# Kernel optimization log

Measured on AMD Instinct MI355X. Metric: run time of the kernel, lower is better.

Reference implementation:

```python
import jax, jax.numpy as jnp
import numpy as np

N_NODES = 50000
N_EDGES = 1200000
F_IN = 128
HID = 64
N_CLASSES = 10
N_GRAPHS = 256
EPS = 1e-5


def setup_inputs() -> dict:
    key = jax.random.key(0)
    ks = jax.random.split(key, 12)
    x = jax.random.normal(ks[0], (N_NODES, F_IN), dtype=jnp.float32)
    edge_index = jax.random.randint(ks[1], (2, N_EDGES), 0, N_NODES, dtype=jnp.int64)
    batch = jnp.sort(jax.random.randint(ks[2], (N_NODES,), 0, N_GRAPHS, dtype=jnp.int64))
    s1 = 1.0 / np.sqrt(F_IN)
    s2 = 1.0 / np.sqrt(HID)
    s3 = 1.0 / np.sqrt(3 * HID)
    return {
        "x": x,
        "edge_index": edge_index,
        "batch": batch,
        "W1": jax.random.normal(ks[3], (F_IN, HID), jnp.float32) * s1,
        "b1": jnp.zeros((HID,), jnp.float32),
        "W2": jax.random.normal(ks[4], (HID, HID), jnp.float32) * s2,  # shared by conv layers 2 and 3
        "b2": jnp.zeros((HID,), jnp.float32),
        "gamma": jnp.ones((HID,), jnp.float32),  # single BatchNorm shared by all 3 layers
        "beta": jnp.zeros((HID,), jnp.float32),
        "lw1": jax.random.normal(ks[5], (3 * HID, HID), jnp.float32) * s3,
        "lb1": jnp.zeros((HID,), jnp.float32),
        "lw2": jax.random.normal(ks[6], (HID, N_CLASSES), jnp.float32) * s2,
        "lb2": jnp.zeros((N_CLASSES,), jnp.float32),
    }


def _batchnorm(h, gamma, beta):
    mu = jnp.mean(h, axis=0)
    var = jnp.mean((h - mu) ** 2, axis=0)  # biased var, training mode
    return (h - mu) * jax.lax.rsqrt(var + EPS) * gamma + beta


def reference(x, edge_index, batch, W1, b1, W2, b2, gamma, beta, lw1, lb1, lw2, lb2):
    src, dst = edge_index[0], edge_index[1]
    # GCN symmetric norm with self-loops: deg includes self-loop weight 1
    deg = jax.ops.segment_sum(jnp.ones((N_EDGES,), x.dtype), dst, num_segments=N_NODES) + 1.0
    dinv = jax.lax.rsqrt(deg)
    coef = dinv[src] * dinv[dst]          # [E]
    self_coef = (dinv * dinv)[:, None]    # [N,1], self-loop contribution

    def gcn_conv(h, W, b):
        h = h @ W
        agg = jax.ops.segment_sum(h[src] * coef[:, None], dst, num_segments=N_NODES)
        return agg + self_coef * h + b

    h = x
    # layer 1 (own weights), layers 2 & 3 share (W2, b2); norm shared across all layers
    h = jax.nn.relu(_batchnorm(gcn_conv(h, W1, b1), gamma, beta))
    h = jax.nn.relu(_batchnorm(gcn_conv(h, W2, b2), gamma, beta))
    h = jax.nn.relu(_batchnorm(gcn_conv(h, W2, b2), gamma, beta))

    # multi-pool: max / mean / add per graph
    pmax = jax.ops.segment_max(h, batch, num_segments=N_GRAPHS)
    pmax = jnp.where(jnp.isfinite(pmax), pmax, 0.0)
    psum = jax.ops.segment_sum(h, batch, num_segments=N_GRAPHS)
    cnt = jax.ops.segment_sum(jnp.ones((N_NODES,), h.dtype), batch, num_segments=N_GRAPHS)
    pmean = psum / jnp.maximum(cnt, 1.0)[:, None]
    emb = jnp.concatenate([pmax, pmean, psum], axis=-1)  # [G, 3H]

    out = jax.nn.relu(emb @ lw1 + lb1) @ lw2 + lb2  # [G, C]
    return out
```

## Files before the change

kernel.cpp:

```cpp
#include <hip/hip_runtime.h>
#include <hip/hip_bf16.h>

#define N_NODES 50000
#define N_EDGES 1200000
#define F_IN 128
#define HID 64
#define N_CLASSES 10
#define N_GRAPHS 256
#define EPSF 1e-5f

#define BSZ 128
#define NB 391
#define BIN_CHUNK 8192

__device__ __forceinline__ float bf2f(unsigned short u) {
    return __uint_as_float((unsigned)u << 16);
}
__device__ __forceinline__ unsigned short f2bf(float f) {
    __hip_bfloat16 h = __float2bfloat16(f);
    return *reinterpret_cast<unsigned short*>(&h);
}


__global__ void k_hist(const int* __restrict__ dst, int* __restrict__ cnt) {
    int e = blockIdx.x * blockDim.x + threadIdx.x;
    if (e < N_EDGES) atomicAdd(&cnt[dst[e]], 1);
}

__global__ __launch_bounds__(1024) void k_scan(const int* __restrict__ cnt,
                                               int* __restrict__ offs,
                                               int* __restrict__ bcur,
                                               float* __restrict__ dinv) {
    __shared__ int wsum[16];
    __shared__ int s_carry;
    int tid = threadIdx.x;
    int lane = tid & 63, wid = tid >> 6;
    if (tid == 0) s_carry = 0;
    __syncthreads();
    for (int base = 0; base < N_NODES; base += 1024) {
        int i = base + tid;
        int v = (i < N_NODES) ? cnt[i] : 0;
        if (i < N_NODES) dinv[i] = rsqrtf((float)v + 1.0f);
        int x = v;
        #pragma unroll
        for (int d = 1; d < 64; d <<= 1) {
            int y = __shfl_up(x, (unsigned)d);
            if (lane >= d) x += y;
        }
        if (lane == 63) wsum[wid] = x;
        __syncthreads();
        if (tid == 0) {
            int run = 0;
            for (int w = 0; w < 16; ++w) { int t = wsum[w]; wsum[w] = run; run += t; }
        }
        __syncthreads();
        int carry = s_carry;
        int excl = carry + wsum[wid] + (x - v);
        if (i < N_NODES) offs[i] = excl;
        __syncthreads();
        if (tid == 1023) s_carry = carry + wsum[15] + x;
        __syncthreads();
    }
    if (tid == 0) offs[N_NODES] = s_carry;
    __syncthreads();
    for (int b = tid; b < NB; b += 1024) bcur[b] = offs[b * BSZ];
}

__global__ __launch_bounds__(256) void k_bin(const int* __restrict__ esrc,
                                             const int* __restrict__ edst,
                                             const float* __restrict__ dinv,
                                             int* __restrict__ bcur,
                                             uint2* __restrict__ binned) {
    __shared__ int lcnt[NB];
    __shared__ int lbase[NB];
    int tid = threadIdx.x;
    for (int i = tid; i < NB; i += 256) lcnt[i] = 0;
    __syncthreads();
    int e0 = blockIdx.x * BIN_CHUNK;
    int myidx[32];
    #pragma unroll
    for (int t = 0; t < 32; ++t) {
        int i = e0 + t * 256 + tid;
        if (i < N_EDGES) {
            int b = edst[i] >> 7;
            int idx = atomicAdd(&lcnt[b], 1);
            myidx[t] = (b << 16) | idx;
        }
    }
    __syncthreads();
    for (int b = tid; b < NB; b += 256)
        if (lcnt[b]) lbase[b] = atomicAdd(&bcur[b], lcnt[b]);
    __syncthreads();
    #pragma unroll
    for (int t = 0; t < 32; ++t) {
        int i = e0 + t * 256 + tid;
        if (i < N_EDGES) {
            int m = myidx[t];
            int b = m >> 16, idx = m & 0xFFFF;
            int s = esrc[i], d = edst[i];
            binned[lbase[b] + idx] =
                make_uint2(((unsigned)d << 16) | (unsigned)s, __float_as_int(dinv[s]));
        }
    }
}

__global__ __launch_bounds__(256) void k_fill2(const uint2* __restrict__ binned,
                                               const int* __restrict__ offs,
                                               unsigned int* __restrict__ csr) {
    __shared__ int cur[BSZ];
    int v0 = blockIdx.x * BSZ;
    int v1 = min(v0 + BSZ, N_NODES);
    int tid = threadIdx.x;
    for (int i = tid; i < BSZ; i += 256)
        cur[i] = (v0 + i < N_NODES) ? offs[v0 + i] : 0;
    __syncthreads();
    int s = offs[v0], e = offs[v1];
    for (int j = s + tid; j < e; j += 256) {
        uint2 E = binned[j];
        int lv = (int)(E.x >> 16) - v0;
        unsigned src = E.x & 0xFFFFu;
        int pos = atomicAdd(&cur[lv], 1);
        csr[pos] = ((unsigned)f2bf(__uint_as_float(E.y)) << 16) | src;
    }
}

__global__ void k_bounds(const int* __restrict__ batch, int* __restrict__ gstart) {
    int v = blockIdx.x * blockDim.x + threadIdx.x;
    if (v >= N_NODES) return;
    if (v == 0) {
        int b = batch[0];
        for (int g = 0; g <= b; ++g) gstart[g] = 0;
    } else {
        int b0 = batch[v - 1], b1 = batch[v];
        for (int g = b0 + 1; g <= b1; ++g) gstart[g] = v;
    }
    if (v == N_NODES - 1) {
        int b = batch[v];
        for (int g = b + 1; g <= N_GRAPHS; ++g) gstart[g] = N_NODES;
    }
}


template <int K, bool NORM>
__global__ __launch_bounds__(256, 2) void k_gemm(const float* __restrict__ A,
                                                 const float* __restrict__ W,
                                                 unsigned short* __restrict__ out_bf,
                                                 const float* __restrict__ stats,
                                                 const float* __restrict__ gamma,
                                                 const float* __restrict__ beta) {
    __shared__ float sW[K * 64];
    __shared__ float sA[32][68];
    __shared__ float ssc[128];
    __shared__ float ssh[128];
    int tid = threadIdx.x;
    for (int i = tid; i < K * 16; i += 256) ((float4*)sW)[i] = ((const float4*)W)[i];
    if (NORM && tid < K) {
        const float invN = 1.0f / (float)N_NODES;
        float mu = stats[tid] * invN;
        float var = stats[64 + tid] * invN - mu * mu;
        float sc = rsqrtf(var + EPSF) * gamma[tid];
        ssc[tid] = sc;
        ssh[tid] = beta[tid] - mu * sc;
    }
    __syncthreads();

    int row0 = blockIdx.x * 64;
    int c0 = (tid & 15) * 4;
    int r0 = (tid >> 4) * 4;
    float acc[4][4] = {};

    #pragma unroll 1
    for (int k0 = 0; k0 < K; k0 += 32) {
        #pragma unroll
        for (int i = 0; i < 2; ++i) {
            int idx = tid + i * 256;
            int row = idx >> 3;
            int kq = idx & 7;
            int grow = row0 + row;
            float4 v = make_float4(0.f, 0.f, 0.f, 0.f);
            if (grow < N_NODES) v = *(const float4*)&A[(size_t)grow * K + k0 + kq * 4];
            if (NORM) {
                int kb = k0 + kq * 4;
                v.x = fmaxf(v.x * ssc[kb + 0] + ssh[kb + 0], 0.f);
                v.y = fmaxf(v.y * ssc[kb + 1] + ssh[kb + 1], 0.f);
                v.z = fmaxf(v.z * ssc[kb + 2] + ssh[kb + 2], 0.f);
                v.w = fmaxf(v.w * ssc[kb + 3] + ssh[kb + 3], 0.f);
            }
            sA[kq * 4 + 0][row] = v.x;
            sA[kq * 4 + 1][row] = v.y;
            sA[kq * 4 + 2][row] = v.z;
            sA[kq * 4 + 3][row] = v.w;
        }
        __syncthreads();
        #pragma unroll 4
        for (int k = 0; k < 32; ++k) {
            float4 a = *(const float4*)&sA[k][r0];
            float4 w = *(const float4*)&sW[(k0 + k) * 64 + c0];
            acc[0][0] += a.x * w.x; acc[0][1] += a.x * w.y; acc[0][2] += a.x * w.z; acc[0][3] += a.x * w.w;
            acc[1][0] += a.y * w.x; acc[1][1] += a.y * w.y; acc[1][2] += a.y * w.z; acc[1][3] += a.y * w.w;
            acc[2][0] += a.z * w.x; acc[2][1] += a.z * w.y; acc[2][2] += a.z * w.z; acc[2][3] += a.z * w.w;
            acc[3][0] += a.w * w.x; acc[3][1] += a.w * w.y; acc[3][2] += a.w * w.z; acc[3][3] += a.w * w.w;
        }
        __syncthreads();
    }
    #pragma unroll
    for (int i = 0; i < 4; ++i) {
        int row = row0 + r0 + i;
        if (row < N_NODES) {
            ushort4 o;
            o.x = f2bf(acc[i][0]); o.y = f2bf(acc[i][1]);
            o.z = f2bf(acc[i][2]); o.w = f2bf(acc[i][3]);
            *(ushort4*)&out_bf[(size_t)row * 64 + c0] = o;
        }
    }
}

__global__ __launch_bounds__(256) void k_agg(const unsigned short* __restrict__ hw,
                                             const int* __restrict__ offs,
                                             const unsigned int* __restrict__ csr,
                                             const float* __restrict__ dinv,
                                             const float* __restrict__ bias,
                                             float* __restrict__ hpre,
                                             float* __restrict__ stats) {
    __shared__ float sred[128];
    if (threadIdx.x < 128) sred[threadIdx.x] = 0.f;
    __syncthreads();
    int lane = threadIdx.x & 63;
    int wave = blockIdx.x * 4 + (threadIdx.x >> 6);
    int nw = gridDim.x * 4;
    float b = bias[lane];
    float lsum = 0.f, lsq = 0.f;
    for (int v = wave; v < N_NODES; v += nw) {
        float dv = dinv[v];
        int s = offs[v], e = offs[v + 1];
        float inner = dv * bf2f(hw[(size_t)v * 64 + lane]);
        int j = s;
        for (; j + 16 <= e; j += 16) {
            unsigned int q[16];
            #pragma unroll
            for (int t = 0; t < 16; ++t) q[t] = csr[j + t];
            float hh[16];
            #pragma unroll
            for (int t = 0; t < 16; ++t)
                hh[t] = bf2f(hw[(size_t)(q[t] & 0xFFFFu) * 64 + lane]);
            #pragma unroll
            for (int t = 0; t < 16; ++t)
                inner += bf2f((unsigned short)(q[t] >> 16)) * hh[t];
        }
        for (; j + 4 <= e; j += 4) {
            unsigned int q0 = csr[j], q1 = csr[j + 1], q2 = csr[j + 2], q3 = csr[j + 3];
            float h0 = bf2f(hw[(size_t)(q0 & 0xFFFFu) * 64 + lane]);
            float h1 = bf2f(hw[(size_t)(q1 & 0xFFFFu) * 64 + lane]);
            float h2 = bf2f(hw[(size_t)(q2 & 0xFFFFu) * 64 + lane]);
            float h3 = bf2f(hw[(size_t)(q3 & 0xFFFFu) * 64 + lane]);
            inner += bf2f((unsigned short)(q0 >> 16)) * h0;
            inner += bf2f((unsigned short)(q1 >> 16)) * h1;
            inner += bf2f((unsigned short)(q2 >> 16)) * h2;
            inner += bf2f((unsigned short)(q3 >> 16)) * h3;
        }
        for (; j < e; ++j) {
            unsigned int q = csr[j];
            inner += bf2f((unsigned short)(q >> 16)) * bf2f(hw[(size_t)(q & 0xFFFFu) * 64 + lane]);
        }
        float acc = dv * inner + b;
        hpre[(size_t)v * 64 + lane] = acc;
        lsum += acc;
        lsq += acc * acc;
    }
    atomicAdd(&sred[lane], lsum);
    atomicAdd(&sred[64 + lane], lsq);
    __syncthreads();
    if (threadIdx.x < 128) atomicAdd(&stats[threadIdx.x], sred[threadIdx.x]);
}

__global__ __launch_bounds__(256) void k_pool(const float* __restrict__ hpre,
                                              const float* __restrict__ stats,
                                              const float* __restrict__ gamma,
                                              const float* __restrict__ beta,
                                              const int* __restrict__ gstart,
                                              const float* __restrict__ lw1,
                                              const float* __restrict__ lb1,
                                              const float* __restrict__ lw2,
                                              const float* __restrict__ lb2,
                                              float* __restrict__ out) {
    __shared__ float smax[4][64];
    __shared__ float ssum[4][64];
    __shared__ float emb[192];
    __shared__ float hid[64];
    int g = blockIdx.x;
    int lane = threadIdx.x & 63;
    int wid = threadIdx.x >> 6;
    int s = gstart[g], e = gstart[g + 1];

    const float invN = 1.0f / (float)N_NODES;
    float mu = stats[lane] * invN;
    float var = stats[64 + lane] * invN - mu * mu;
    float sc = rsqrtf(var + EPSF) * gamma[lane];
    float sh = beta[lane] - mu * sc;

    float mx = 0.f, sm = 0.f;
    for (int v = s + wid; v < e; v += 4) {
        float h = fmaxf(hpre[(size_t)v * 64 + lane] * sc + sh, 0.f);
        mx = fmaxf(mx, h);
        sm += h;
    }
    smax[wid][lane] = mx;
    ssum[wid][lane] = sm;
    __syncthreads();
    if (wid == 0) {
        float m = fmaxf(fmaxf(smax[0][lane], smax[1][lane]), fmaxf(smax[2][lane], smax[3][lane]));
        float su = ssum[0][lane] + ssum[1][lane] + ssum[2][lane] + ssum[3][lane];
        float inv = 1.0f / fmaxf((float)(e - s), 1.0f);
        emb[lane] = m;
        emb[64 + lane] = su * inv;
        emb[128 + lane] = su;
    }
    __syncthreads();
    if (wid == 0) {
        float acc = lb1[lane];
        #pragma unroll 4
        for (int k = 0; k < 192; ++k) acc += emb[k] * lw1[k * 64 + lane];
        hid[lane] = fmaxf(acc, 0.f);
    }
    __syncthreads();
    if (threadIdx.x < N_CLASSES) {
        int j = threadIdx.x;
        float o = lb2[j];
        #pragma unroll 8
        for (int k = 0; k < 64; ++k) o += hid[k] * lw2[k * 10 + j];
        out[(size_t)g * 10 + j] = o;
    }
}


extern "C" void kernel_launch(void* const* d_in, const int* in_sizes, int n_in,
                              void* d_out, int out_size, void* d_ws, size_t ws_size,
                              hipStream_t stream) {
    const float* x     = (const float*)d_in[0];
    const int* eidx    = (const int*)d_in[1];
    const int* batch   = (const int*)d_in[2];
    const float* W1    = (const float*)d_in[3];
    const float* b1    = (const float*)d_in[4];
    const float* W2    = (const float*)d_in[5];
    const float* b2    = (const float*)d_in[6];
    const float* gamma = (const float*)d_in[7];
    const float* beta  = (const float*)d_in[8];
    const float* lw1   = (const float*)d_in[9];
    const float* lb1   = (const float*)d_in[10];
    const float* lw2   = (const float*)d_in[11];
    const float* lb2   = (const float*)d_in[12];
    float* out = (float*)d_out;

    const int* e_src = eidx;
    const int* e_dst = eidx + N_EDGES;

    char* p = (char*)d_ws;
    auto carve = [&](size_t bytes) { char* r = p; p += (bytes + 255) & ~(size_t)255; return r; };
    int*   cnt   = (int*)carve((size_t)N_NODES * 4);
    float* stats = (float*)carve(3 * 128 * 4);
    size_t zero_bytes = (size_t)(p - (char*)d_ws);
    int*   offs   = (int*)carve((size_t)(N_NODES + 1) * 4);
    int*   bcur   = (int*)carve((size_t)NB * 4);
    float* dinv   = (float*)carve((size_t)N_NODES * 4);
    int*   gstart = (int*)carve((size_t)(N_GRAPHS + 1) * 4);
    uint2* binned = (uint2*)carve((size_t)N_EDGES * 8);
    unsigned int* csr = (unsigned int*)carve((size_t)N_EDGES * 4);
    unsigned short* B0 = (unsigned short*)carve((size_t)N_NODES * 64 * 2);
    float* B1     = (float*)carve((size_t)N_NODES * 64 * 4);

    hipMemsetAsync(d_ws, 0, zero_bytes, stream);

    k_hist<<<(N_EDGES + 255) / 256, 256, 0, stream>>>(e_dst, cnt);
    k_scan<<<1, 1024, 0, stream>>>(cnt, offs, bcur, dinv);
    k_bin<<<(N_EDGES + BIN_CHUNK - 1) / BIN_CHUNK, 256, 0, stream>>>(e_src, e_dst, dinv, bcur, binned);
    k_fill2<<<NB, 256, 0, stream>>>(binned, offs, csr);
    k_bounds<<<(N_NODES + 255) / 256, 256, 0, stream>>>(batch, gstart);

    const int GEMM_GRID = (N_NODES + 63) / 64;
    k_gemm<128, false><<<GEMM_GRID, 256, 0, stream>>>(x, W1, B0, nullptr, nullptr, nullptr);
    k_agg<<<2048, 256, 0, stream>>>(B0, offs, csr, dinv, b1, B1, stats);
    k_gemm<64, true><<<GEMM_GRID, 256, 0, stream>>>(B1, W2, B0, stats, gamma, beta);
    k_agg<<<2048, 256, 0, stream>>>(B0, offs, csr, dinv, b2, B1, stats + 128);
    k_gemm<64, true><<<GEMM_GRID, 256, 0, stream>>>(B1, W2, B0, stats + 128, gamma, beta);
    k_agg<<<2048, 256, 0, stream>>>(B0, offs, csr, dinv, b2, B1, stats + 256);
    k_pool<<<N_GRAPHS, 256, 0, stream>>>(B1, stats + 256, gamma, beta, gstart,
                                         lw1, lb1, lw2, lb2, out);
}
```

Before: 534.2 us.

## Split wave into 4 edge groups with vectorized ushort4 feature gathers in aggregation

The aggregation kernel now lets each 16-lane group of a wave handle a different edge, with each lane loading four bf16 features as one ushort4. The four partial sums are then combined with cross-lane shuffles. This means four edges are gathered per wave instruction and each lane issues fewer, wider loads. The tail loops are replaced by clamped, masked loads, which cost some wasted work on short rows, and only one quarter of the lanes write output and statistics.

```diff
diff --git a/kernel.cpp b/kernel.cpp
--- a/kernel.cpp
+++ b/kernel.cpp
@@ -226,49 +226,60 @@
     if (threadIdx.x < 128) sred[threadIdx.x] = 0.f;
     __syncthreads();
     int lane = threadIdx.x & 63;
+    int fq = lane & 15;
+    int eg = lane >> 4;
     int wave = blockIdx.x * 4 + (threadIdx.x >> 6);
     int nw = gridDim.x * 4;
-    float b = bias[lane];
-    float lsum = 0.f, lsq = 0.f;
+    const ushort4* hw4 = (const ushort4*)hw;
+    float4 b4 = *(const float4*)&bias[fq * 4];
+    float sx = 0.f, sy = 0.f, sz = 0.f, sw = 0.f;
+    float qx = 0.f, qy = 0.f, qz = 0.f, qw = 0.f;
     for (int v = wave; v < N_NODES; v += nw) {
         float dv = dinv[v];
         int s = offs[v], e = offs[v + 1];
-        float inner = dv * bf2f(hw[(size_t)v * 64 + lane]);
-        int j = s;
-        for (; j + 16 <= e; j += 16) {
-            unsigned int q[16];
+        float ax = 0.f, ay = 0.f, az = 0.f, aw = 0.f;
+        for (int j = s; j < e; j += 16) {
             #pragma unroll
-            for (int t = 0; t < 16; ++t) q[t] = csr[j + t];
-            float hh[16];
-            #pragma unroll
-            for (int t = 0; t < 16; ++t)
-                hh[t] = bf2f(hw[(size_t)(q[t] & 0xFFFFu) * 64 + lane]);
-            #pragma unroll
-            for (int t = 0; t < 16; ++t)
-                inner += bf2f((unsigned short)(q[t] >> 16)) * hh[t];
-        }
-        for (; j + 4 <= e; j += 4) {
-            unsigned int q0 = csr[j], q1 = csr[j + 1], q2 = csr[j + 2], q3 = csr[j + 3];
-            float h0 = bf2f(hw[(size_t)(q0 & 0xFFFFu) * 64 + lane]);
-            float h1 = bf2f(hw[(size_t)(q1 & 0xFFFFu) * 64 + lane]);
-            float h2 = bf2f(hw[(size_t)(q2 & 0xFFFFu) * 64 + lane]);
-            float h3 = bf2f(hw[(size_t)(q3 & 0xFFFFu) * 64 + lane]);
-            inner += bf2f((unsigned short)(q0 >> 16)) * h0;
-            inner += bf2f((unsigned short)(q1 >> 16)) * h1;
-            inner += bf2f((unsigned short)(q2 >> 16)) * h2;
-            inner += bf2f((unsigned short)(q3 >> 16)) * h3;
-        }
-        for (; j < e; ++j) {
-            unsigned int q = csr[j];
-            inner += bf2f((unsigned short)(q >> 16)) * bf2f(hw[(size_t)(q & 0xFFFFu) * 64 + lane]);
-        }
-        float acc = dv * inner + b;
-        hpre[(size_t)v * 64 + lane] = acc;
-        lsum += acc;
-        lsq += acc * acc;
-    }
-    atomicAdd(&sred[lane], lsum);
-    atomicAdd(&sred[64 + lane], lsq);
+            for (int t = 0; t < 4; ++t) {
+                int idx = j + 4 * t + eg;
+                unsigned q = csr[min(idx, e - 1)];
+                float w = __uint_as_float(q & 0xFFFF0000u);
+                w = (idx < e) ? w : 0.f;
+                ushort4 h = hw4[(size_t)(q & 0xFFFFu) * 16 + fq];
+                ax += w * bf2f(h.x);
+                ay += w * bf2f(h.y);
+                az += w * bf2f(h.z);
+                aw += w * bf2f(h.w);
+            }
+        }
+        #pragma unroll
+        for (int m = 16; m < 64; m <<= 1) {
+            ax += __shfl_xor(ax, m);
+            ay += __shfl_xor(ay, m);
+            az += __shfl_xor(az, m);
+            aw += __shfl_xor(aw, m);
+        }
+        ushort4 hv = hw4[(size_t)v * 16 + fq];
+        float dv2 = dv * dv;
+        float rx = dv * ax + dv2 * bf2f(hv.x) + b4.x;
+        float ry = dv * ay + dv2 * bf2f(hv.y) + b4.y;
+        float rz = dv * az + dv2 * bf2f(hv.z) + b4.z;
+        float rw = dv * aw + dv2 * bf2f(hv.w) + b4.w;
+        if (lane < 16)
+            *(float4*)&hpre[(size_t)v * 64 + fq * 4] = make_float4(rx, ry, rz, rw);
+        sx += rx; sy += ry; sz += rz; sw += rw;
+        qx += rx * rx; qy += ry * ry; qz += rz * rz; qw += rw * rw;
+    }
+    if (lane < 16) {
+        atomicAdd(&sred[4 * fq + 0], sx);
+        atomicAdd(&sred[4 * fq + 1], sy);
+        atomicAdd(&sred[4 * fq + 2], sz);
+        atomicAdd(&sred[4 * fq + 3], sw);
+        atomicAdd(&sred[64 + 4 * fq + 0], qx);
+        atomicAdd(&sred[64 + 4 * fq + 1], qy);
+        atomicAdd(&sred[64 + 4 * fq + 2], qz);
+        atomicAdd(&sred[64 + 4 * fq + 3], qw);
+    }
     __syncthreads();
     if (threadIdx.x < 128) atomicAdd(&stats[threadIdx.x], sred[threadIdx.x]);
 }
```

New measurement: 520.0 us. -2.7%, faster.
